# Kernel tuning notes

Measured on AMD Instinct MI355X. Metric: run time of the kernel, lower is better.

## Reference

```python
import jax, jax.numpy as jnp
import numpy as np

N_NODES = 100000
N_EDGES = 1200000


def gcn_conv(h, W, b, src, dst, n_nodes):
    """PyG GCNConv: h' = D^-1/2 (A+I) D^-1/2 (h W) + b, with self-loops."""
    h = h @ W  # [N, out]
    # degree on A + I (count of incoming edges at dst, plus self-loop)
    deg = jnp.zeros((n_nodes,), h.dtype).at[dst].add(1.0) + 1.0
    dis = jax.lax.rsqrt(deg)  # deg^-1/2, deg >= 1 so safe
    norm = dis[src] * dis[dst]  # [E]
    out = jnp.zeros_like(h).at[dst].add(norm[:, None] * h[src])
    out = out + (1.0 / deg)[:, None] * h  # self-loop term: dis_i^2 * h_i
    return out + b


def global_features(x, T_norm):
    # matches compute_global_features; torch uses .item() so these are constants
    n_comp = jnp.sum(x[:, 2])
    n_AND = jnp.sum(x[:, 3])
    n_OR = jnp.sum(x[:, 4])
    mask = (x[:, 2] == 1.0).astype(x.dtype)
    msum = jnp.sum(mask)
    safe = jnp.maximum(msum, 1.0)
    avg_lambda = jnp.where(msum > 0, jnp.sum(x[:, 0] * mask) / safe, 0.0)
    avg_mu = jnp.where(msum > 0, jnp.sum(x[:, 1] * mask) / safe, 0.0)
    depth = n_AND + n_OR
    g = jnp.stack([n_comp, n_AND, n_OR, depth, avg_lambda, avg_mu, T_norm])[None, :]
    return jax.lax.stop_gradient(g)


def setup_inputs() -> dict:
    key = jax.random.key(0)
    ks = jax.random.split(key, 8)
    x = jax.random.normal(ks[0], (N_NODES, 5), jnp.float32)
    edge_index = jax.random.randint(ks[1], (2, N_EDGES), 0, N_NODES, jnp.int64)
    sc = lambda f: 1.0 / np.sqrt(f)
    return {
        "x": x,
        "edge_index": edge_index,
        "W1": jax.random.normal(ks[2], (5, 64), jnp.float32) * sc(5),
        "b1": jnp.zeros((64,), jnp.float32),
        "W2": jax.random.normal(ks[3], (64, 64), jnp.float32) * sc(64),
        "b2": jnp.zeros((64,), jnp.float32),
        "Wp1": jax.random.normal(ks[4], (71, 32), jnp.float32) * sc(71),
        "bp1": jnp.zeros((32,), jnp.float32),
        "Wp2": jax.random.normal(ks[5], (32, 2), jnp.float32) * sc(32),
        "bp2": jnp.zeros((2,), jnp.float32),
        "T": 100,
        "T_max": 500,
    }


def reference(x, edge_index, W1, b1, W2, b2, Wp1, bp1, Wp2, bp2, T, T_max):
    src, dst = edge_index[0], edge_index[1]
    n = x.shape[0]
    h = jax.nn.relu(gcn_conv(x, W1, b1, src, dst, n))
    h = jax.nn.relu(gcn_conv(h, W2, b2, src, dst, n))
    embedding = jnp.mean(h, axis=0, keepdims=True)  # global_mean_pool, single graph
    T_norm = jnp.asarray(T, x.dtype) / jnp.asarray(T_max, x.dtype)
    g = global_features(x, T_norm)
    e = jnp.concatenate([embedding, g], axis=1)  # [1, 71]
    raw = jax.nn.relu(e @ Wp1 + bp1) @ Wp2 + bp2  # [1, 2]
    return 2.0 + jax.nn.sigmoid(raw) * 4.0
```

## Files before the change

### kernel.cpp

```cpp
#include <hip/hip_runtime.h>
#include <hip/hip_bf16.h>

#define N_NODES_C 100000
#define N_EDGES_C 1200000
#define NB2 98
#define SUBCAP2 1792

typedef unsigned int uint32;
typedef __attribute__((ext_vector_type(8))) short bf16x8;
typedef __attribute__((ext_vector_type(4))) float f32x4;
typedef __attribute__((ext_vector_type(2))) float f32x2;

__device__ __forceinline__ float bf_lo(uint32 u) { return __uint_as_float(u << 16); }
__device__ __forceinline__ float bf_hi(uint32 u) { return __uint_as_float(u & 0xffff0000u); }
__device__ __forceinline__ uint32 bf16r(float f) {
    uint32 u = __float_as_uint(f);
    return (u + 0x7fffu + ((u >> 16) & 1u)) >> 16;
}
__device__ __forceinline__ uint32 pack2(float lo, float hi) {
    return bf16r(lo) | (bf16r(hi) << 16);
}

__global__ void bucket_kernel(const int4* __restrict__ src4, const int4* __restrict__ dst4,
                              int* __restrict__ bcnt, uint32* __restrict__ bedges, int nE4) {
    __shared__ int cntL[NB2];
    __shared__ int baseL[NB2];
    int tid = threadIdx.x;
    int i = blockIdx.x * 256 + tid;
    int sub = blockIdx.x & 7;
    for (int t = tid; t < NB2; t += 256) cntL[t] = 0;
    __syncthreads();
    int4 s4 = make_int4(0, 0, 0, 0), d4 = make_int4(0, 0, 0, 0);
    int b0 = 0, b1 = 0, b2 = 0, b3 = 0;
    bool act = i < nE4;
    if (act) {
        s4 = src4[i];
        d4 = dst4[i];
        b0 = d4.x >> 10; b1 = d4.y >> 10; b2 = d4.z >> 10; b3 = d4.w >> 10;
        atomicAdd(&cntL[b0], 1); atomicAdd(&cntL[b1], 1);
        atomicAdd(&cntL[b2], 1); atomicAdd(&cntL[b3], 1);
    }
    __syncthreads();
    for (int t = tid; t < NB2; t += 256) {
        int n = cntL[t];
        baseL[t] = n ? atomicAdd(&bcnt[sub * NB2 + t], n) : 0;
    }
    __syncthreads();
    for (int t = tid; t < NB2; t += 256) cntL[t] = 0;
    __syncthreads();
    if (act) {
        int o, slot;
        o = atomicAdd(&cntL[b0], 1); slot = baseL[b0] + o;
        if (slot < SUBCAP2)
            bedges[((size_t)b0 * 8 + sub) * SUBCAP2 + slot] =
                (uint32)s4.x | ((uint32)(d4.x & 1023) << 17);
        o = atomicAdd(&cntL[b1], 1); slot = baseL[b1] + o;
        if (slot < SUBCAP2)
            bedges[((size_t)b1 * 8 + sub) * SUBCAP2 + slot] =
                (uint32)s4.y | ((uint32)(d4.y & 1023) << 17);
        o = atomicAdd(&cntL[b2], 1); slot = baseL[b2] + o;
        if (slot < SUBCAP2)
            bedges[((size_t)b2 * 8 + sub) * SUBCAP2 + slot] =
                (uint32)s4.z | ((uint32)(d4.z & 1023) << 17);
        o = atomicAdd(&cntL[b3], 1); slot = baseL[b3] + o;
        if (slot < SUBCAP2)
            bedges[((size_t)b3 * 8 + sub) * SUBCAP2 + slot] =
                (uint32)s4.w | ((uint32)(d4.w & 1023) << 17);
    }
}

__global__ void cnt2_kernel(const uint32* __restrict__ bedges, const int* __restrict__ bcnt,
                            int* __restrict__ cnt, int nN) {
    __shared__ int lc[1024];
    __shared__ int ln[8];
    int b = blockIdx.x;
    int tid = threadIdx.x;
    lc[tid] = 0;
    if (tid < 8) ln[tid] = min(bcnt[tid * NB2 + b], SUBCAP2);
    __syncthreads();
    const uint32* be = bedges + (size_t)b * 8 * SUBCAP2;
#pragma unroll
    for (int s = 0; s < 8; ++s) {
        int n = ln[s];
        const uint32* bs = be + s * SUBCAP2;
        for (int i = tid; i < n; i += 1024) atomicAdd(&lc[bs[i] >> 17], 1);
    }
    __syncthreads();
    int node = b * 1024 + tid;
    if (node < nN) cnt[node] = lc[tid];
}

__global__ void bsum_kernel(const int* __restrict__ cnt, int* __restrict__ bsum, int nN) {
    __shared__ int sm[256];
    int tid = threadIdx.x;
    int base = blockIdx.x * 1024 + tid * 4;
    int s = 0;
#pragma unroll
    for (int k = 0; k < 4; ++k)
        if (base + k < nN) s += cnt[base + k];
    sm[tid] = s;
    __syncthreads();
    for (int off = 128; off > 0; off >>= 1) {
        if (tid < off) sm[tid] += sm[tid + off];
        __syncthreads();
    }
    if (tid == 0) bsum[blockIdx.x] = sm[0];
}

__global__ void bscan_kernel(const int* __restrict__ bsum, int* __restrict__ boff, int nb) {
    __shared__ int sm[128];
    int tid = threadIdx.x;
    sm[tid] = (tid < nb) ? bsum[tid] : 0;
    __syncthreads();
    for (int off = 1; off < 128; off <<= 1) {
        int t = (tid >= off) ? sm[tid - off] : 0;
        __syncthreads();
        sm[tid] += t;
        __syncthreads();
    }
    if (tid < nb) boff[tid] = (tid ? sm[tid - 1] : 0);
}

__global__ void scan_block_kernel(const int* __restrict__ cnt, const int* __restrict__ boff,
                                  int* __restrict__ rowptr, float* __restrict__ dis, int nN) {
    __shared__ int sm[256];
    int tid = threadIdx.x;
    int base = blockIdx.x * 1024 + tid * 4;
    int v0 = 0, v1 = 0, v2 = 0, v3 = 0;
    if (base + 0 < nN) v0 = cnt[base + 0];
    if (base + 1 < nN) v1 = cnt[base + 1];
    if (base + 2 < nN) v2 = cnt[base + 2];
    if (base + 3 < nN) v3 = cnt[base + 3];
    int tsum = v0 + v1 + v2 + v3;
    sm[tid] = tsum;
    __syncthreads();
    for (int off = 1; off < 256; off <<= 1) {
        int t = (tid >= off) ? sm[tid - off] : 0;
        __syncthreads();
        sm[tid] += t;
        __syncthreads();
    }
    int excl = (tid ? sm[tid - 1] : 0) + boff[blockIdx.x];
    if (base + 0 <= nN) rowptr[base + 0] = excl;
    if (base + 1 <= nN) rowptr[base + 1] = excl + v0;
    if (base + 2 <= nN) rowptr[base + 2] = excl + v0 + v1;
    if (base + 3 <= nN) rowptr[base + 3] = excl + v0 + v1 + v2;
    if (base + 0 < nN) dis[base + 0] = rsqrtf((float)(v0 + 1));
    if (base + 1 < nN) dis[base + 1] = rsqrtf((float)(v1 + 1));
    if (base + 2 < nN) dis[base + 2] = rsqrtf((float)(v2 + 1));
    if (base + 3 < nN) dis[base + 3] = rsqrtf((float)(v3 + 1));
}

__global__ void bin2_kernel(const uint32* __restrict__ bedges, const int* __restrict__ bcnt,
                            const int* __restrict__ rowptr, int* __restrict__ csr_src) {
    __shared__ int lfill[1024];
    __shared__ int ln[8];
    int b = blockIdx.x;
    int tid = threadIdx.x;
    lfill[tid] = 0;
    if (tid < 8) ln[tid] = min(bcnt[tid * NB2 + b], SUBCAP2);
    __syncthreads();
    const uint32* be = bedges + (size_t)b * 8 * SUBCAP2;
    int nodeBase = b << 10;
#pragma unroll
    for (int s = 0; s < 8; ++s) {
        int n = ln[s];
        const uint32* bs = be + s * SUBCAP2;
        for (int i = tid; i < n; i += 1024) {
            uint32 ed = bs[i];
            int dlow = ed >> 17;
            int slot = rowptr[nodeBase + dlow] + atomicAdd(&lfill[dlow], 1);
            csr_src[slot] = ed & 0x1FFFF;
        }
    }
}

__global__ void lin1_kernel(const float* __restrict__ x, const float* __restrict__ W1,
                            const float* __restrict__ dis, uint32* __restrict__ hlin, int nN) {
    __shared__ float Ws[320];
    int tid = threadIdx.x;
    if (tid < 256) Ws[tid] = W1[tid];
    if (tid < 64)  Ws[256 + tid] = W1[256 + tid];
    __syncthreads();
    int q = tid & 15;
    int sub = tid >> 4;
    for (int node = blockIdx.x * 16 + sub; node < nN; node += gridDim.x * 16) {
        const float* xr = x + node * 5;
        float x0 = xr[0], x1 = xr[1], x2 = xr[2], x3 = xr[3], x4 = xr[4];
        float dn = dis[node];
        int j = 4 * q;
        float a0 = x0 * Ws[j+0] + x1 * Ws[64+j+0] + x2 * Ws[128+j+0] + x3 * Ws[192+j+0] + x4 * Ws[256+j+0];
        float a1 = x0 * Ws[j+1] + x1 * Ws[64+j+1] + x2 * Ws[128+j+1] + x3 * Ws[192+j+1] + x4 * Ws[256+j+1];
        float a2 = x0 * Ws[j+2] + x1 * Ws[64+j+2] + x2 * Ws[128+j+2] + x3 * Ws[192+j+2] + x4 * Ws[256+j+2];
        float a3 = x0 * Ws[j+3] + x1 * Ws[64+j+3] + x2 * Ws[128+j+3] + x3 * Ws[192+j+3] + x4 * Ws[256+j+3];
        uint32 w = 0;
        w = __builtin_amdgcn_cvt_pk_fp8_f32(a0 * dn, a1 * dn, w, 0);
        w = __builtin_amdgcn_cvt_pk_fp8_f32(a2 * dn, a3 * dn, w, 1);
        hlin[node * 16 + q] = w;
    }
}

template <bool EPI>
__global__ void gather_kernel(const int* __restrict__ rowptr, const int* __restrict__ csr_src,
                              const uint2* __restrict__ hin, const float* __restrict__ bias,
                              void* __restrict__ hout, int nN) {
    int tid = threadIdx.x;
    int lane = tid & 63;
    int wv = tid >> 6;
    int g = lane >> 3;
    int l = lane & 7;
    float bb0 = 0, bb1 = 0, bb2 = 0, bb3 = 0, bb4 = 0, bb5 = 0, bb6 = 0, bb7 = 0;
    if (EPI) {
        const float* bp = bias + 8 * l;
        bb0 = bp[0]; bb1 = bp[1]; bb2 = bp[2]; bb3 = bp[3];
        bb4 = bp[4]; bb5 = bp[5]; bb6 = bp[6]; bb7 = bp[7];
    }
    int stride = gridDim.x * 32;
    for (int node = blockIdx.x * 32 + wv * 8 + g; node < nN; node += stride) {
        int e0 = rowptr[node];
        int e1 = rowptr[node + 1];
        float a0 = 0, a1 = 0, a2 = 0, a3 = 0, a4 = 0, a5 = 0, a6 = 0, a7 = 0;
        int e = e0;
        for (; e + 2 <= e1; e += 2) {
            int s0 = csr_src[e];
            int s1 = csr_src[e + 1];
            uint2 h0 = hin[(size_t)s0 * 8 + l];
            uint2 h1 = hin[(size_t)s1 * 8 + l];
            f32x2 p0 = __builtin_amdgcn_cvt_pk_f32_fp8(h0.x, 0);
            f32x2 p1 = __builtin_amdgcn_cvt_pk_f32_fp8(h0.x, 1);
            f32x2 p2 = __builtin_amdgcn_cvt_pk_f32_fp8(h0.y, 0);
            f32x2 p3 = __builtin_amdgcn_cvt_pk_f32_fp8(h0.y, 1);
            f32x2 q0 = __builtin_amdgcn_cvt_pk_f32_fp8(h1.x, 0);
            f32x2 q1 = __builtin_amdgcn_cvt_pk_f32_fp8(h1.x, 1);
            f32x2 q2 = __builtin_amdgcn_cvt_pk_f32_fp8(h1.y, 0);
            f32x2 q3 = __builtin_amdgcn_cvt_pk_f32_fp8(h1.y, 1);
            a0 += p0.x + q0.x; a1 += p0.y + q0.y;
            a2 += p1.x + q1.x; a3 += p1.y + q1.y;
            a4 += p2.x + q2.x; a5 += p2.y + q2.y;
            a6 += p3.x + q3.x; a7 += p3.y + q3.y;
        }
        if (e < e1) {
            int s0 = csr_src[e];
            uint2 h0 = hin[(size_t)s0 * 8 + l];
            f32x2 p0 = __builtin_amdgcn_cvt_pk_f32_fp8(h0.x, 0);
            f32x2 p1 = __builtin_amdgcn_cvt_pk_f32_fp8(h0.x, 1);
            f32x2 p2 = __builtin_amdgcn_cvt_pk_f32_fp8(h0.y, 0);
            f32x2 p3 = __builtin_amdgcn_cvt_pk_f32_fp8(h0.y, 1);
            a0 += p0.x; a1 += p0.y; a2 += p1.x; a3 += p1.y;
            a4 += p2.x; a5 += p2.y; a6 += p3.x; a7 += p3.y;
        }
        float dn = rsqrtf((float)(e1 - e0 + 1));
        uint2 hs = hin[(size_t)node * 8 + l];
        {
            f32x2 p0 = __builtin_amdgcn_cvt_pk_f32_fp8(hs.x, 0);
            f32x2 p1 = __builtin_amdgcn_cvt_pk_f32_fp8(hs.x, 1);
            f32x2 p2 = __builtin_amdgcn_cvt_pk_f32_fp8(hs.y, 0);
            f32x2 p3 = __builtin_amdgcn_cvt_pk_f32_fp8(hs.y, 1);
            a0 = (a0 + p0.x) * dn; a1 = (a1 + p0.y) * dn;
            a2 = (a2 + p1.x) * dn; a3 = (a3 + p1.y) * dn;
            a4 = (a4 + p2.x) * dn; a5 = (a5 + p2.y) * dn;
            a6 = (a6 + p3.x) * dn; a7 = (a7 + p3.y) * dn;
        }
        if (EPI) {
            a0 = fmaxf(a0 + bb0, 0.0f) * dn; a1 = fmaxf(a1 + bb1, 0.0f) * dn;
            a2 = fmaxf(a2 + bb2, 0.0f) * dn; a3 = fmaxf(a3 + bb3, 0.0f) * dn;
            a4 = fmaxf(a4 + bb4, 0.0f) * dn; a5 = fmaxf(a5 + bb5, 0.0f) * dn;
            a6 = fmaxf(a6 + bb6, 0.0f) * dn; a7 = fmaxf(a7 + bb7, 0.0f) * dn;
            uint32 w0 = 0, w1 = 0;
            w0 = __builtin_amdgcn_cvt_pk_fp8_f32(a0, a1, w0, 0);
            w0 = __builtin_amdgcn_cvt_pk_fp8_f32(a2, a3, w0, 1);
            w1 = __builtin_amdgcn_cvt_pk_fp8_f32(a4, a5, w1, 0);
            w1 = __builtin_amdgcn_cvt_pk_fp8_f32(a6, a7, w1, 1);
            ((uint2*)hout)[(size_t)node * 8 + l] = make_uint2(w0, w1);
        } else {
            ((uint4*)hout)[(size_t)node * 8 + l] = make_uint4(pack2(a0, a1), pack2(a2, a3),
                                                              pack2(a4, a5), pack2(a6, a7));
        }
    }
}

__global__ void lin2pool_kernel(const uint2* __restrict__ z2, const float* __restrict__ W2,
                                const float* __restrict__ b2, float* __restrict__ colsumB,
                                int nTiles) {
    int tid = threadIdx.x;
    int lane = tid & 63;
    int wv = tid >> 6;
    int l16 = lane & 15;
    int kg = lane >> 4;

    bf16x8 Bf[2][4];
#pragma unroll
    for (int ks = 0; ks < 2; ++ks)
#pragma unroll
        for (int t = 0; t < 4; ++t) {
            bf16x8 bb;
#pragma unroll
            for (int r = 0; r < 8; ++r) {
                int k = ks * 32 + kg * 8 + r;
                bb[r] = (short)bf16r(W2[k * 64 + t * 16 + l16]);
            }
            Bf[ks][t] = bb;
        }
    float bbias[4];
#pragma unroll
    for (int t = 0; t < 4; ++t) bbias[t] = b2[t * 16 + l16];

    float colacc[4][4];
#pragma unroll
    for (int t = 0; t < 4; ++t)
#pragma unroll
        for (int r = 0; r < 4; ++r) colacc[t][r] = 0.0f;

    for (int tile = blockIdx.x * 4 + wv; tile < nTiles; tile += gridDim.x * 4) {
        int nodeBase = tile * 16;
        const uint4* zrow = (const uint4*)(z2 + (size_t)(nodeBase + l16) * 16);
        uint4 A0u = zrow[kg];
        uint4 A1u = zrow[4 + kg];
        union { uint4 u; bf16x8 b; } c0, c1;
        c0.u = A0u; c1.u = A1u;
        f32x4 acc0 = {0, 0, 0, 0}, acc1 = {0, 0, 0, 0}, acc2 = {0, 0, 0, 0}, acc3 = {0, 0, 0, 0};
        acc0 = __builtin_amdgcn_mfma_f32_16x16x32_bf16(c0.b, Bf[0][0], acc0, 0, 0, 0);
        acc1 = __builtin_amdgcn_mfma_f32_16x16x32_bf16(c0.b, Bf[0][1], acc1, 0, 0, 0);
        acc2 = __builtin_amdgcn_mfma_f32_16x16x32_bf16(c0.b, Bf[0][2], acc2, 0, 0, 0);
        acc3 = __builtin_amdgcn_mfma_f32_16x16x32_bf16(c0.b, Bf[0][3], acc3, 0, 0, 0);
        acc0 = __builtin_amdgcn_mfma_f32_16x16x32_bf16(c1.b, Bf[1][0], acc0, 0, 0, 0);
        acc1 = __builtin_amdgcn_mfma_f32_16x16x32_bf16(c1.b, Bf[1][1], acc1, 0, 0, 0);
        acc2 = __builtin_amdgcn_mfma_f32_16x16x32_bf16(c1.b, Bf[1][2], acc2, 0, 0, 0);
        acc3 = __builtin_amdgcn_mfma_f32_16x16x32_bf16(c1.b, Bf[1][3], acc3, 0, 0, 0);
#pragma unroll
        for (int r = 0; r < 4; ++r) {
            colacc[0][r] += fmaxf(acc0[r] + bbias[0], 0.0f);
            colacc[1][r] += fmaxf(acc1[r] + bbias[1], 0.0f);
            colacc[2][r] += fmaxf(acc2[r] + bbias[2], 0.0f);
            colacc[3][r] += fmaxf(acc3[r] + bbias[3], 0.0f);
        }
    }
    float s[4];
#pragma unroll
    for (int t = 0; t < 4; ++t) {
        s[t] = colacc[t][0] + colacc[t][1] + colacc[t][2] + colacc[t][3];
        s[t] += __shfl_down(s[t], 32);
        s[t] += __shfl_down(s[t], 16);
    }
    __shared__ float sm[4][64];
    if (lane < 16) {
#pragma unroll
        for (int t = 0; t < 4; ++t) sm[wv][t * 16 + lane] = s[t];
    }
    __syncthreads();
    if (tid < 64) {
        float v = sm[0][tid] + sm[1][tid] + sm[2][tid] + sm[3][tid];
        atomicAdd(&colsumB[(blockIdx.x & 15) * 64 + tid], v);
    }
}

__global__ void gfeat_kernel(const float* __restrict__ x, float* __restrict__ gsB, int nN) {
    int tid = threadIdx.x;
    int i = blockIdx.x * 256 + tid;
    float s0 = 0, s1 = 0, s2 = 0, s3 = 0, s4 = 0, s5 = 0;
    if (i < nN) {
        const float* xr = x + i * 5;
        float x0 = xr[0], x1 = xr[1], x2 = xr[2], x3 = xr[3], x4 = xr[4];
        float m = (x2 == 1.0f) ? 1.0f : 0.0f;
        s0 = x0 * m; s1 = x1 * m; s2 = x2; s3 = x3; s4 = x4; s5 = m;
    }
#pragma unroll
    for (int off = 32; off > 0; off >>= 1) {
        s0 += __shfl_down(s0, off);
        s1 += __shfl_down(s1, off);
        s2 += __shfl_down(s2, off);
        s3 += __shfl_down(s3, off);
        s4 += __shfl_down(s4, off);
        s5 += __shfl_down(s5, off);
    }
    __shared__ float smg[4][6];
    if ((tid & 63) == 0) {
        int w = tid >> 6;
        smg[w][0] = s0; smg[w][1] = s1; smg[w][2] = s2;
        smg[w][3] = s3; smg[w][4] = s4; smg[w][5] = s5;
    }
    __syncthreads();
    if (tid < 6) {
        float s = smg[0][tid] + smg[1][tid] + smg[2][tid] + smg[3][tid];
        atomicAdd(&gsB[(blockIdx.x & 15) * 16 + tid], s);
    }
}

__global__ void head_kernel(const float* __restrict__ colsumB, const float* __restrict__ gsB,
                            const float* __restrict__ Wp1, const float* __restrict__ bp1,
                            const float* __restrict__ Wp2, const float* __restrict__ bp2,
                            const int* __restrict__ T, const int* __restrict__ Tmax,
                            float* __restrict__ out) {
    __shared__ float e[71];
    __shared__ float gsum[6];
    __shared__ float hid[32];
    int tid = threadIdx.x;
    if (tid < 64) {
        float s = 0.0f;
#pragma unroll
        for (int r = 0; r < 16; ++r) s += colsumB[r * 64 + tid];
        e[tid] = s * (1.0f / (float)N_NODES_C);
    } else if (tid < 70) {
        int k = tid - 64;
        float s = 0.0f;
#pragma unroll
        for (int r = 0; r < 16; ++r) s += gsB[r * 16 + k];
        gsum[k] = s;
    }
    __syncthreads();
    if (tid == 0) {
        e[64] = gsum[2];
        e[65] = gsum[3];
        e[66] = gsum[4];
        e[67] = gsum[3] + gsum[4];
        float m = gsum[5];
        e[68] = (m > 0.0f) ? gsum[0] / fmaxf(m, 1.0f) : 0.0f;
        e[69] = (m > 0.0f) ? gsum[1] / fmaxf(m, 1.0f) : 0.0f;
        e[70] = (float)T[0] / (float)Tmax[0];
    }
    __syncthreads();
    if (tid < 32) {
        float acc = bp1[tid];
        for (int i = 0; i < 71; ++i) acc += e[i] * Wp1[i * 32 + tid];
        hid[tid] = fmaxf(acc, 0.0f);
    }
    __syncthreads();
    if (tid < 2) {
        float acc = bp2[tid];
        for (int k = 0; k < 32; ++k) acc += hid[k] * Wp2[k * 2 + tid];
        out[tid] = 2.0f + 4.0f / (1.0f + expf(-acc));
    }
}

extern "C" void kernel_launch(void* const* d_in, const int* in_sizes, int n_in,
                              void* d_out, int out_size, void* d_ws, size_t ws_size,
                              hipStream_t stream) {
    const float* x    = (const float*)d_in[0];
    const int*   ei   = (const int*)d_in[1];
    const float* W1   = (const float*)d_in[2];
    const float* b1   = (const float*)d_in[3];
    const float* W2   = (const float*)d_in[4];
    const float* b2   = (const float*)d_in[5];
    const float* Wp1  = (const float*)d_in[6];
    const float* bp1  = (const float*)d_in[7];
    const float* Wp2  = (const float*)d_in[8];
    const float* bp2  = (const float*)d_in[9];
    const int*   T    = (const int*)d_in[10];
    const int*   Tmax = (const int*)d_in[11];
    float* out = (float*)d_out;

    const int nN = N_NODES_C;
    const int nE = N_EDGES_C;
    const int* src = ei;
    const int* dst = ei + nE;

    char* ws = (char*)d_ws;
    int*    bcnt    = (int*)   (ws + 0);
    float*  colsumB = (float*) (ws + 3136);
    float*  gsB     = (float*) (ws + 7232);
    int*    bsum    = (int*)   (ws + 8256);
    int*    boff    = (int*)   (ws + 8768);
    int*    cnt     = (int*)   (ws + 9280);
    int*    rowptr  = (int*)   (ws + 409280);
    float*  dis     = (float*) (ws + 809296);
    int*    csr_src = (int*)   (ws + 1209296);
    uint32* bedges  = (uint32*)(ws + 6009296);
    uint32* hlin1   = (uint32*)(ws + 11629008);
    uint32* h1      = (uint32*)(ws + 18029008);
    uint32* z2      = (uint32*)(ws + 24429008);

    hipMemsetAsync(ws, 0, 8256, stream);

    const int nb = (nN + 1023) / 1024;

    bucket_kernel<<<(nE / 4 + 255) / 256, 256, 0, stream>>>(
        (const int4*)src, (const int4*)dst, bcnt, bedges, nE / 4);
    cnt2_kernel<<<NB2, 1024, 0, stream>>>(bedges, bcnt, cnt, nN);
    bsum_kernel<<<nb, 256, 0, stream>>>(cnt, bsum, nN);
    bscan_kernel<<<1, 128, 0, stream>>>(bsum, boff, nb);
    scan_block_kernel<<<nb, 256, 0, stream>>>(cnt, boff, rowptr, dis, nN);
    bin2_kernel<<<NB2, 1024, 0, stream>>>(bedges, bcnt, rowptr, csr_src);

    lin1_kernel<<<1024, 256, 0, stream>>>(x, W1, dis, hlin1, nN);
    gather_kernel<true><<<2048, 256, 0, stream>>>(rowptr, csr_src, (const uint2*)hlin1, b1,
                                                  (void*)h1, nN);

    gather_kernel<false><<<2048, 256, 0, stream>>>(rowptr, csr_src, (const uint2*)h1, nullptr,
                                                   (void*)z2, nN);
    lin2pool_kernel<<<512, 256, 0, stream>>>((const uint2*)z2, W2, b2, colsumB, nN / 16);

    gfeat_kernel<<<(nN + 255) / 256, 256, 0, stream>>>(x, gsB, nN);

    head_kernel<<<1, 128, 0, stream>>>(colsumB, gsB, Wp1, bp1, Wp2, bp2, T, Tmax, out);
}
```

Measured before the change: 189.4 us.

## Fuse CSR count, scan and binning into one per-bucket kernel

Replaces the five CSR-construction kernels (cnt2, bsum, bscan, scan_block, bin2) with two. A small kernel derives per-bucket offsets directly from the bucket counts, and one 1024-thread block per bucket then counts, scans, writes rowptr and dis, and scatters csr_src using offsets held in shared memory. This removes three launches and the global round-trip through cnt and rowptr, and it frees the cnt and bsum workspace. In exchange it adds a longer in-block scan with more barriers and more shared memory per block. Bucket offsets now use uncapped bucket counts, so they would diverge from the capped per-bucket data only if a sub-bucket overflowed.

New measurement: 184.0 us. 1.03x faster.

```diff
diff --git a/kernel.cpp b/kernel.cpp
--- a/kernel.cpp
+++ b/kernel.cpp
@@ -69,9 +69,32 @@
     }
 }
 
-__global__ void cnt2_kernel(const uint32* __restrict__ bedges, const int* __restrict__ bcnt,
-                            int* __restrict__ cnt, int nN) {
+__global__ void bscan2_kernel(const int* __restrict__ bcnt, int* __restrict__ boff) {
+    __shared__ int sm[128];
+    int tid = threadIdx.x;
+    int t = 0;
+    if (tid < NB2) {
+#pragma unroll
+        for (int s = 0; s < 8; ++s) t += bcnt[s * NB2 + tid];
+    }
+    sm[tid] = t;
+    __syncthreads();
+    for (int off = 1; off < 128; off <<= 1) {
+        int v = (tid >= off) ? sm[tid - off] : 0;
+        __syncthreads();
+        sm[tid] += v;
+        __syncthreads();
+    }
+    if (tid < NB2) boff[tid] = sm[tid] - t;
+}
+
+__global__ void __launch_bounds__(1024)
+bin3_kernel(const uint32* __restrict__ bedges, const int* __restrict__ bcnt,
+            const int* __restrict__ boff, int* __restrict__ rowptr,
+            float* __restrict__ dis, int* __restrict__ csr_src, int nN) {
     __shared__ int lc[1024];
+    __shared__ int sm[1024];
+    __shared__ int pr[1024];
     __shared__ int ln[8];
     int b = blockIdx.x;
     int tid = threadIdx.x;
@@ -86,82 +109,23 @@
         for (int i = tid; i < n; i += 1024) atomicAdd(&lc[bs[i] >> 17], 1);
     }
     __syncthreads();
-    int node = b * 1024 + tid;
-    if (node < nN) cnt[node] = lc[tid];
-}
-
-__global__ void bsum_kernel(const int* __restrict__ cnt, int* __restrict__ bsum, int nN) {
-    __shared__ int sm[256];
-    int tid = threadIdx.x;
-    int base = blockIdx.x * 1024 + tid * 4;
-    int s = 0;
-#pragma unroll
-    for (int k = 0; k < 4; ++k)
-        if (base + k < nN) s += cnt[base + k];
-    sm[tid] = s;
-    __syncthreads();
-    for (int off = 128; off > 0; off >>= 1) {
-        if (tid < off) sm[tid] += sm[tid + off];
+    int myc = lc[tid];
+    sm[tid] = myc;
+    __syncthreads();
+    for (int off = 1; off < 1024; off <<= 1) {
+        int v = (tid >= off) ? sm[tid - off] : 0;
         __syncthreads();
-    }
-    if (tid == 0) bsum[blockIdx.x] = sm[0];
-}
-
-__global__ void bscan_kernel(const int* __restrict__ bsum, int* __restrict__ boff, int nb) {
-    __shared__ int sm[128];
-    int tid = threadIdx.x;
-    sm[tid] = (tid < nb) ? bsum[tid] : 0;
-    __syncthreads();
-    for (int off = 1; off < 128; off <<= 1) {
-        int t = (tid >= off) ? sm[tid - off] : 0;
+        sm[tid] += v;
         __syncthreads();
-        sm[tid] += t;
-        __syncthreads();
-    }
-    if (tid < nb) boff[tid] = (tid ? sm[tid - 1] : 0);
-}
-
-__global__ void scan_block_kernel(const int* __restrict__ cnt, const int* __restrict__ boff,
-                                  int* __restrict__ rowptr, float* __restrict__ dis, int nN) {
-    __shared__ int sm[256];
-    int tid = threadIdx.x;
-    int base = blockIdx.x * 1024 + tid * 4;
-    int v0 = 0, v1 = 0, v2 = 0, v3 = 0;
-    if (base + 0 < nN) v0 = cnt[base + 0];
-    if (base + 1 < nN) v1 = cnt[base + 1];
-    if (base + 2 < nN) v2 = cnt[base + 2];
-    if (base + 3 < nN) v3 = cnt[base + 3];
-    int tsum = v0 + v1 + v2 + v3;
-    sm[tid] = tsum;
-    __syncthreads();
-    for (int off = 1; off < 256; off <<= 1) {
-        int t = (tid >= off) ? sm[tid - off] : 0;
-        __syncthreads();
-        sm[tid] += t;
-        __syncthreads();
-    }
-    int excl = (tid ? sm[tid - 1] : 0) + boff[blockIdx.x];
-    if (base + 0 <= nN) rowptr[base + 0] = excl;
-    if (base + 1 <= nN) rowptr[base + 1] = excl + v0;
-    if (base + 2 <= nN) rowptr[base + 2] = excl + v0 + v1;
-    if (base + 3 <= nN) rowptr[base + 3] = excl + v0 + v1 + v2;
-    if (base + 0 < nN) dis[base + 0] = rsqrtf((float)(v0 + 1));
-    if (base + 1 < nN) dis[base + 1] = rsqrtf((float)(v1 + 1));
-    if (base + 2 < nN) dis[base + 2] = rsqrtf((float)(v2 + 1));
-    if (base + 3 < nN) dis[base + 3] = rsqrtf((float)(v3 + 1));
-}
-
-__global__ void bin2_kernel(const uint32* __restrict__ bedges, const int* __restrict__ bcnt,
-                            const int* __restrict__ rowptr, int* __restrict__ csr_src) {
-    __shared__ int lfill[1024];
-    __shared__ int ln[8];
-    int b = blockIdx.x;
-    int tid = threadIdx.x;
-    lfill[tid] = 0;
-    if (tid < 8) ln[tid] = min(bcnt[tid * NB2 + b], SUBCAP2);
-    __syncthreads();
-    const uint32* be = bedges + (size_t)b * 8 * SUBCAP2;
-    int nodeBase = b << 10;
+    }
+    int excl = sm[tid] - myc;
+    int base = boff[b];
+    pr[tid] = base + excl;
+    int node = (b << 10) + tid;
+    if (node <= nN) rowptr[node] = base + excl;
+    if (node < nN) dis[node] = rsqrtf((float)(myc + 1));
+    lc[tid] = 0;
+    __syncthreads();
 #pragma unroll
     for (int s = 0; s < 8; ++s) {
         int n = ln[s];
@@ -169,7 +133,7 @@
         for (int i = tid; i < n; i += 1024) {
             uint32 ed = bs[i];
             int dlow = ed >> 17;
-            int slot = rowptr[nodeBase + dlow] + atomicAdd(&lfill[dlow], 1);
+            int slot = pr[dlow] + atomicAdd(&lc[dlow], 1);
             csr_src[slot] = ed & 0x1FFFF;
         }
     }
@@ -458,28 +422,21 @@
     int*    bcnt    = (int*)   (ws + 0);
     float*  colsumB = (float*) (ws + 3136);
     float*  gsB     = (float*) (ws + 7232);
-    int*    bsum    = (int*)   (ws + 8256);
-    int*    boff    = (int*)   (ws + 8768);
-    int*    cnt     = (int*)   (ws + 9280);
-    int*    rowptr  = (int*)   (ws + 409280);
-    float*  dis     = (float*) (ws + 809296);
-    int*    csr_src = (int*)   (ws + 1209296);
-    uint32* bedges  = (uint32*)(ws + 6009296);
-    uint32* hlin1   = (uint32*)(ws + 11629008);
-    uint32* h1      = (uint32*)(ws + 18029008);
-    uint32* z2      = (uint32*)(ws + 24429008);
+    int*    boff    = (int*)   (ws + 8256);
+    int*    rowptr  = (int*)   (ws + 8768);
+    float*  dis     = (float*) (ws + 408784);
+    int*    csr_src = (int*)   (ws + 808784);
+    uint32* bedges  = (uint32*)(ws + 5608784);
+    uint32* hlin1   = (uint32*)(ws + 11228496);
+    uint32* h1      = (uint32*)(ws + 17628496);
+    uint32* z2      = (uint32*)(ws + 24028496);
 
     hipMemsetAsync(ws, 0, 8256, stream);
-
-    const int nb = (nN + 1023) / 1024;
 
     bucket_kernel<<<(nE / 4 + 255) / 256, 256, 0, stream>>>(
         (const int4*)src, (const int4*)dst, bcnt, bedges, nE / 4);
-    cnt2_kernel<<<NB2, 1024, 0, stream>>>(bedges, bcnt, cnt, nN);
-    bsum_kernel<<<nb, 256, 0, stream>>>(cnt, bsum, nN);
-    bscan_kernel<<<1, 128, 0, stream>>>(bsum, boff, nb);
-    scan_block_kernel<<<nb, 256, 0, stream>>>(cnt, boff, rowptr, dis, nN);
-    bin2_kernel<<<NB2, 1024, 0, stream>>>(bedges, bcnt, rowptr, csr_src);
+    bscan2_kernel<<<1, 128, 0, stream>>>(bcnt, boff);
+    bin3_kernel<<<NB2, 1024, 0, stream>>>(bedges, bcnt, boff, rowptr, dis, csr_src, nN);
 
     lin1_kernel<<<1024, 256, 0, stream>>>(x, W1, dis, hlin1, nN);
     gather_kernel<true><<<2048, 256, 0, stream>>>(rowptr, csr_src, (const uint2*)hlin1, b1,
```
